# Optimization experiments

Hardware: AMD Instinct MI355X
Metric: run time of the kernel (lower is better)

Reference implementation:

```python
import jax, jax.numpy as jnp
import numpy as np
import math

N_HEAD = 8
LN_EPS = 1e-5


def _layernorm(x, w, b):
    # Biased variance as in the triton kernel: var = E[x^2] - mean^2
    mean = jnp.mean(x, axis=-1, keepdims=True)
    var = jnp.mean(x * x, axis=-1, keepdims=True) - mean * mean
    return (x - mean) * jax.lax.rsqrt(var + LN_EPS) * w + b


def _gelu_tanh(x):
    # matches triton gelu: tanh approximation
    return 0.5 * x * (1.0 + jnp.tanh(0.7978845608 * (x + 0.044715 * x * x * x)))


def _causal_attention(qkv, n_head):
    B, T, C3 = qkv.shape
    C = C3 // 3
    D = C // n_head
    q, k, v = jnp.split(qkv, 3, axis=-1)
    q = q.reshape(B, T, n_head, D)
    k = k.reshape(B, T, n_head, D)
    v = v.reshape(B, T, n_head, D)
    scale = 1.0 / math.sqrt(D)
    scores = jnp.einsum('bqhd,bkhd->bhqk', q, k) * scale  # [B,H,T,T]
    causal = jnp.tril(jnp.ones((T, T), dtype=bool))
    scores = jnp.where(causal, scores, -jnp.inf)
    p = jax.nn.softmax(scores, axis=-1)
    out = jnp.einsum('bhqk,bkhd->bqhd', p, v)
    return out.reshape(B, T, C)


def setup_inputs() -> dict:
    key = jax.random.key(0)
    ks = jax.random.split(key, 8)
    B, T, C = 8, 2048, 768
    s = 0.02
    return {
        'x': jax.random.normal(ks[0], (B, T, C), jnp.float32),
        'ln1_w': jnp.ones((C,), jnp.float32),
        'ln1_b': jnp.zeros((C,), jnp.float32),
        'w_qkv': jax.random.normal(ks[1], (3 * C, C), jnp.float32) * s,
        'b_qkv': jnp.zeros((3 * C,), jnp.float32),
        'w_attn_proj': jax.random.normal(ks[2], (C, C), jnp.float32) * s,
        'b_attn_proj': jnp.zeros((C,), jnp.float32),
        'ln2_w': jnp.ones((C,), jnp.float32),
        'ln2_b': jnp.zeros((C,), jnp.float32),
        'w_fc': jax.random.normal(ks[3], (4 * C, C), jnp.float32) * s,
        'b_fc': jnp.zeros((4 * C,), jnp.float32),
        'w_mlp_proj': jax.random.normal(ks[4], (C, 4 * C), jnp.float32) * s,
        'b_mlp_proj': jnp.zeros((C,), jnp.float32),
    }


def reference(x, ln1_w, ln1_b, w_qkv, b_qkv, w_attn_proj, b_attn_proj,
              ln2_w, ln2_b, w_fc, b_fc, w_mlp_proj, b_mlp_proj):
    # attention block: fused LN + QKV linear, causal flash attention, out proj, residual
    qkv = _layernorm(x, ln1_w, ln1_b) @ w_qkv.T + b_qkv          # [B,T,3C]
    att = _causal_attention(qkv, N_HEAD)                          # [B,T,C]
    x = x + (att @ w_attn_proj.T + b_attn_proj)
    # MLP block: fused LN + fc + gelu, proj, residual
    h = _gelu_tanh(_layernorm(x, ln2_w, ln2_b) @ w_fc.T + b_fc)   # [B,T,4C]
    x = x + (h @ w_mlp_proj.T + b_mlp_proj)
    return x
```

## Files before the change

kernel.cpp:

```cpp
#include <hip/hip_runtime.h>
#include <hip/hip_bf16.h>
#include <cstdint>
#include <cstddef>

typedef __attribute__((ext_vector_type(8))) short bf16x8;
typedef __attribute__((ext_vector_type(4))) short bf16x4;
typedef __attribute__((ext_vector_type(4))) float f32x4;
typedef __attribute__((ext_vector_type(16))) float f32x16;

#define GLB_AS(p) ((const __attribute__((address_space(1))) void*)(p))
#define LDS_AS(p) ((__attribute__((address_space(3))) void*)(p))

__device__ __forceinline__ short f2bf(float f) {
    union { float f; unsigned u; } x; x.f = f;
    unsigned r = (x.u + 0x7fffu + ((x.u >> 16) & 1u)) >> 16;
    return (short)r;
}
__device__ __forceinline__ float bf2f(short s) {
    union { unsigned u; float f; } x;
    x.u = ((unsigned)(unsigned short)s) << 16;
    return x.f;
}
__device__ __forceinline__ unsigned packbf2(float a, float b) {
    union { float f; unsigned u; } x, y; x.f = a; y.f = b;
    return (x.u >> 16) | (y.u & 0xffff0000u);
}
__device__ __forceinline__ f32x4 MF(bf16x8 a, bf16x8 b, f32x4 c) {
    return __builtin_amdgcn_mfma_f32_16x16x32_bf16(a, b, c, 0, 0, 0);
}
__device__ __forceinline__ f32x16 MF32(bf16x8 a, bf16x8 b, f32x16 c) {
    return __builtin_amdgcn_mfma_f32_32x32x16_bf16(a, b, c, 0, 0, 0);
}

__global__ __launch_bounds__(256) void k_prep(const float* __restrict__ x,
                                              const float* __restrict__ ln1_w,
                                              const float* __restrict__ ln1_b,
                                              short* __restrict__ xhat,
                                              const float* __restrict__ s0,
                                              const float* __restrict__ s1,
                                              const float* __restrict__ s2,
                                              const float* __restrict__ s3,
                                              short* __restrict__ d0,
                                              short* __restrict__ d1,
                                              short* __restrict__ d2,
                                              short* __restrict__ d3,
                                              int n0, int n1, int n2, int n3) {
    const int row = blockIdx.x;
    const int tid = threadIdx.x;
    {
        const float* xr = x + (size_t)row * 768;
        float v0 = xr[tid], v1 = xr[tid + 256], v2 = xr[tid + 512];
        float s = v0 + v1 + v2;
        float ss = v0 * v0 + v1 * v1 + v2 * v2;
        #pragma unroll
        for (int m = 32; m; m >>= 1) { s += __shfl_xor(s, m); ss += __shfl_xor(ss, m); }
        __shared__ float red[8];
        int wid = tid >> 6, lane = tid & 63;
        if (lane == 0) { red[wid] = s; red[4 + wid] = ss; }
        __syncthreads();
        s = red[0] + red[1] + red[2] + red[3];
        ss = red[4] + red[5] + red[6] + red[7];
        float mean = s * (1.f / 768.f);
        float var = ss * (1.f / 768.f) - mean * mean;
        float inv = rsqrtf(var + 1e-5f);
        short* orow = xhat + (size_t)row * 768;
        orow[tid]       = f2bf((v0 - mean) * inv * ln1_w[tid]       + ln1_b[tid]);
        orow[tid + 256] = f2bf((v1 - mean) * inv * ln1_w[tid + 256] + ln1_b[tid + 256]);
        orow[tid + 512] = f2bf((v2 - mean) * inv * ln1_w[tid + 512] + ln1_b[tid + 512]);
    }
    const int total = n0 + n1 + n2 + n3;
    const int stride = gridDim.x * 256;
    for (int i = blockIdx.x * 256 + tid; i < total; i += stride) {
        int j = i;
        const float* s; short* d;
        if (j < n0) { s = s0; d = d0; }
        else {
            j -= n0;
            if (j < n1) { s = s1; d = d1; }
            else {
                j -= n1;
                if (j < n2) { s = s2; d = d2; }
                else { j -= n2; s = s3; d = d3; }
            }
        }
        float4 v = ((const float4*)s)[j];
        bf16x4 o;
        o[0] = f2bf(v.x); o[1] = f2bf(v.y); o[2] = f2bf(v.z); o[3] = f2bf(v.w);
        ((bf16x4*)d)[j] = o;
    }
}

__global__ __launch_bounds__(256) void k_layernorm_bf(const short* __restrict__ xb,
                                                      const float* __restrict__ w,
                                                      const float* __restrict__ b,
                                                      short* __restrict__ out) {
    const int row = blockIdx.x;
    const int tid = threadIdx.x;
    float v[4] = {0.f, 0.f, 0.f, 0.f};
    if (tid < 192) {
        bf16x4 raw = ((const bf16x4*)(xb + (size_t)row * 768))[tid];
        #pragma unroll
        for (int j = 0; j < 4; ++j) v[j] = bf2f(raw[j]);
    }
    float s = v[0] + v[1] + v[2] + v[3];
    float ss = v[0] * v[0] + v[1] * v[1] + v[2] * v[2] + v[3] * v[3];
    #pragma unroll
    for (int m = 32; m; m >>= 1) { s += __shfl_xor(s, m); ss += __shfl_xor(ss, m); }
    __shared__ float red[8];
    int wid = tid >> 6, lane = tid & 63;
    if (lane == 0) { red[wid] = s; red[4 + wid] = ss; }
    __syncthreads();
    s = red[0] + red[1] + red[2] + red[3];
    ss = red[4] + red[5] + red[6] + red[7];
    float mean = s * (1.f / 768.f);
    float var = ss * (1.f / 768.f) - mean * mean;
    float inv = rsqrtf(var + 1e-5f);
    if (tid < 192) {
        float4 wv = ((const float4*)w)[tid];
        float4 bv = ((const float4*)b)[tid];
        bf16x4 o;
        o[0] = f2bf((v[0] - mean) * inv * wv.x + bv.x);
        o[1] = f2bf((v[1] - mean) * inv * wv.y + bv.y);
        o[2] = f2bf((v[2] - mean) * inv * wv.z + bv.z);
        o[3] = f2bf((v[3] - mean) * inv * wv.w + bv.w);
        ((bf16x4*)(out + (size_t)row * 768))[tid] = o;
    }
}

template <int EPI, int NFR>
__global__ __launch_bounds__(512, 2) void k_gemm256(const short* __restrict__ A,
                                                    const short* __restrict__ B,
                                                    const float* __restrict__ bias,
                                                    const void* __restrict__ res,
                                                    void* __restrict__ out,
                                                    int M, int N, int K) {
    __shared__ short As2[2][256 * 64];
    __shared__ short Bs2[2][NFR * 64 * 64];
    const int tid = threadIdx.x, lane = tid & 63, wid = tid >> 6;
    const int l4 = lane & 15, lh = lane >> 4;
    const int wm = wid >> 2, wn = wid & 3;
    const int gx = gridDim.x;
    const int nwg = gx * gridDim.y;
    int wg = blockIdx.y * gx + blockIdx.x;
    { const int q = nwg >> 3; wg = (wg & 7) * q + (wg >> 3); }
    const int row0 = (wg / gx) * 256, col0 = (wg % gx) * (NFR * 64);

    auto stageA = [&](short* lds, int mh, int k0) {
        #pragma unroll
        for (int i = 0; i < 2; ++i) {
            const int chunk = wid * 2 + i;
            const int dl = mh * 16384 + chunk * 1024 + lane * 16;
            const int r = dl >> 7;
            const int cb = (dl & 127) ^ ((r & 7) << 4);
            __builtin_amdgcn_global_load_lds(
                GLB_AS(A + (size_t)(row0 + r) * K + k0 + (cb >> 1)),
                LDS_AS(lds + mh * 8192 + chunk * 512), 16, 0, 0);
        }
    };
    auto stageB = [&](short* lds, int k0) {
        #pragma unroll
        for (int i = 0; i < NFR; ++i) {
            const int chunk = wid * NFR + i;
            const int dl = chunk * 1024 + lane * 16;
            const int r = dl >> 7;
            const int cb = (dl & 127) ^ ((r & 7) << 4);
            __builtin_amdgcn_global_load_lds(
                GLB_AS(B + (size_t)(col0 + r) * K + k0 + (cb >> 1)),
                LDS_AS(lds + chunk * 512), 16, 0, 0);
        }
    };
    auto rd = [&](const short* lds, int r, int kb) -> bf16x8 {
        return *(const bf16x8*)((const char*)lds + r * 128 +
                                ((kb * 64 + lh * 16) ^ ((r & 7) << 4)));
    };

    f32x4 acc[8][NFR] = {};
    bf16x8 a[4][2], b0[2][2], b1[2][2];
    const int NT = K >> 6;

    stageA(As2[0], 0, 0);
    stageA(As2[0], 1, 0);
    stageB(Bs2[0], 0);
    asm volatile("s_waitcnt vmcnt(0)" ::: "memory");
    __builtin_amdgcn_s_barrier();

    for (int t = 0; t < NT; ++t) {
        const int cur = t & 1, nxt = cur ^ 1;
        const short* Ac = As2[cur];
        const short* Bc = Bs2[cur];
        const int kn = (t + 1) << 6;
        const bool more = (t + 1 < NT);
        #pragma unroll
        for (int mi = 0; mi < 4; ++mi) {
            const int r = wm * 128 + mi * 16 + l4;
            a[mi][0] = rd(Ac, r, 0); a[mi][1] = rd(Ac, r, 1);
        }
        #pragma unroll
        for (int ni = 0; ni < 2; ++ni) {
            const int r = wn * (NFR * 16) + ni * 16 + l4;
            b0[ni][0] = rd(Bc, r, 0); b0[ni][1] = rd(Bc, r, 1);
        }
        if (more) { stageA(As2[nxt], 0, kn); stageA(As2[nxt], 1, kn); }
        __builtin_amdgcn_s_setprio(1);
        #pragma unroll
        for (int mi = 0; mi < 4; ++mi)
            #pragma unroll
            for (int ni = 0; ni < 2; ++ni) {
                acc[mi][ni] = MF(a[mi][0], b0[ni][0], acc[mi][ni]);
                acc[mi][ni] = MF(a[mi][1], b0[ni][1], acc[mi][ni]);
            }
        __builtin_amdgcn_s_setprio(0);
        __builtin_amdgcn_s_barrier();
        #pragma unroll
        for (int j = 0; j < NFR - 2; ++j) {
            const int r = wn * (NFR * 16) + (2 + j) * 16 + l4;
            b1[j][0] = rd(Bc, r, 0); b1[j][1] = rd(Bc, r, 1);
        }
        if (more) stageB(Bs2[nxt], kn);
        __builtin_amdgcn_s_setprio(1);
        #pragma unroll
        for (int mi = 0; mi < 4; ++mi)
            #pragma unroll
            for (int j = 0; j < NFR - 2; ++j) {
                acc[mi][2 + j] = MF(a[mi][0], b1[j][0], acc[mi][2 + j]);
                acc[mi][2 + j] = MF(a[mi][1], b1[j][1], acc[mi][2 + j]);
            }
        __builtin_amdgcn_s_setprio(0);
        __builtin_amdgcn_s_barrier();
        #pragma unroll
        for (int mi = 0; mi < 4; ++mi) {
            const int r = wm * 128 + (4 + mi) * 16 + l4;
            a[mi][0] = rd(Ac, r, 0); a[mi][1] = rd(Ac, r, 1);
        }
        __builtin_amdgcn_s_setprio(1);
        #pragma unroll
        for (int mi = 0; mi < 4; ++mi)
            #pragma unroll
            for (int j = 0; j < NFR - 2; ++j) {
                acc[4 + mi][2 + j] = MF(a[mi][0], b1[j][0], acc[4 + mi][2 + j]);
                acc[4 + mi][2 + j] = MF(a[mi][1], b1[j][1], acc[4 + mi][2 + j]);
            }
        __builtin_amdgcn_s_setprio(0);
        __builtin_amdgcn_s_barrier();
        __builtin_amdgcn_s_setprio(1);
        #pragma unroll
        for (int mi = 0; mi < 4; ++mi)
            #pragma unroll
            for (int ni = 0; ni < 2; ++ni) {
                acc[4 + mi][ni] = MF(a[mi][0], b0[ni][0], acc[4 + mi][ni]);
                acc[4 + mi][ni] = MF(a[mi][1], b0[ni][1], acc[4 + mi][ni]);
            }
        __builtin_amdgcn_s_setprio(0);
        if (more) asm volatile("s_waitcnt vmcnt(0)" ::: "memory");
        __builtin_amdgcn_s_barrier();
    }

    #pragma unroll
    for (int mi = 0; mi < 8; ++mi) {
        const int rowb = row0 + wm * 128 + mi * 16 + lh * 4;
        #pragma unroll
        for (int ni = 0; ni < NFR; ++ni) {
            const int col = col0 + wn * (NFR * 16) + ni * 16 + l4;
            const float bv = bias[col];
            #pragma unroll
            for (int j = 0; j < 4; ++j) {
                const size_t idx = (size_t)(rowb + j) * N + col;
                float v = acc[mi][ni][j] + bv;
                if (EPI == 0) {
                    ((short*)out)[idx] = f2bf(v);
                } else if (EPI == 2) {
                    float u = v + 0.044715f * v * v * v;
                    float t = 1.f - 2.f / (__expf(1.5957691216f * u) + 1.f);
                    ((short*)out)[idx] = f2bf(0.5f * v * (1.f + t));
                } else if (EPI == 3) {
                    ((short*)out)[idx] = f2bf(v + ((const float*)res)[idx]);
                } else {
                    ((float*)out)[idx] = v + bf2f(((const short*)res)[idx]);
                }
            }
        }
    }
}

#define ATTN_PROC(QF, O, LROW, QA, Q0)                                         \
    if (kv0 <= (Q0) + 31) {                                                    \
        const bool full = (kv0 + 63 <= (Q0));                                  \
        f32x16 s0 = {}, s1 = {};                                               \
        __builtin_amdgcn_s_setprio(1);                                         \
        _Pragma("unroll")                                                      \
        for (int kb = 0; kb < 6; ++kb) {                                       \
            const int r0 = lq, r1 = 32 + lq;                                   \
            bf16x8 kf0 = *(const bf16x8*)((const char*)&Ks[cur][0] +           \
                          r0 * 256 + ((kb * 32 + hi * 16) ^ ((r0 & 7) << 4))); \
            bf16x8 kf1 = *(const bf16x8*)((const char*)&Ks[cur][0] +           \
                          r1 * 256 + ((kb * 32 + hi * 16) ^ ((r1 & 7) << 4))); \
            s0 = MF32(kf0, QF[kb], s0);                                        \
            s1 = MF32(kf1, QF[kb], s1);                                        \
        }                                                                      \
        __builtin_amdgcn_s_setprio(0);                                         \
        if (!full) {                                                           \
            _Pragma("unroll")                                                  \
            for (int r = 0; r < 16; ++r) {                                     \
                const int kvl = (r & 3) + 8 * (r >> 2) + 4 * hi;               \
                if (kv0 + kvl > (QA)) s0[r] = -INFINITY;                       \
                if (kv0 + 32 + kvl > (QA)) s1[r] = -INFINITY;                  \
            }                                                                  \
        }                                                                      \
        _Pragma("unroll")                                                      \
        for (int r = 0; r < 16; ++r) { s0[r] = exp2f(s0[r]); s1[r] = exp2f(s1[r]); } \
        float ar[16];                                                          \
        _Pragma("unroll")                                                      \
        for (int r = 0; r < 16; ++r) ar[r] = s0[r] + s1[r];                    \
        _Pragma("unroll")                                                      \
        for (int st = 8; st; st >>= 1)                                         \
            _Pragma("unroll")                                                  \
            for (int r = 0; r < 8; ++r)                                        \
                if (r < st) ar[r] += ar[r + st];                               \
        (LROW) += ar[0] + __shfl_xor(ar[0], 32);                               \
        unsigned pk0[8], pk1[8];                                               \
        _Pragma("unroll")                                                      \
        for (int j = 0; j < 8; ++j) {                                          \
            pk0[j] = packbf2(s0[2 * j], s0[2 * j + 1]);                        \
            pk1[j] = packbf2(s1[2 * j], s1[2 * j + 1]);                        \
        }                                                                      \
        __builtin_amdgcn_s_setprio(1);                                         \
        _Pragma("unroll")                                                      \
        for (int db = 0; db < 3; ++db) {                                       \
            const int vrow = db * 32 + lq;                                     \
            const int vsw = ((vrow & 7) ^ ((vrow >> 3) & 7)) << 4;             \
            _Pragma("unroll")                                                  \
            for (int c = 0; c < 4; ++c) {                                      \
                bf16x8 vf = *(const bf16x8*)((const char*)&Vs[cur][0] +        \
                             vrow * 128 + ((c * 32 + hi * 16) ^ vsw));         \
                union { unsigned u[4]; bf16x8 v; } pa;                         \
                const unsigned* pk = (c < 2) ? pk0 : pk1;                      \
                const int o4 = (c & 1) * 4;                                    \
                pa.u[0] = pk[o4]; pa.u[1] = pk[o4 + 1];                        \
                pa.u[2] = pk[o4 + 2]; pa.u[3] = pk[o4 + 3];                    \
                (O)[db] = MF32(vf, pa.v, (O)[db]);                             \
            }                                                                  \
        }                                                                      \
        __builtin_amdgcn_s_setprio(0);                                         \
    }

__global__ __launch_bounds__(256, 2) void k_attn8(const short* __restrict__ qkv,
                                                  short* __restrict__ att) {
    __shared__ short Ks[2][64 * 128];
    __shared__ short Vs[2][96 * 64];
    const int tid = threadIdx.x, lane = tid & 63, wid = tid >> 6;
    const int lq = lane & 31, hi = lane >> 5;
    const int L = blockIdx.x;
    const int h = L & 7, bx = (L >> 3) & 7, b = L >> 6;
    const short* base = qkv + (size_t)b * 2048 * 2304 + h * 96;
    const short* Kb = base + 768;
    const short* Vb = base + 1536;
    const int vkvr = (tid / 12) * 4, vd0 = (tid % 12) * 8;
    const int vslot = (vkvr & ~12) | ((vkvr & 4) << 1) | ((vkvr & 8) >> 1);
    bf16x8 vreg[4];
    const float QSC = 0.14724445f;

    auto stageK = [&](int jt, int bb) {
        const int kv0 = jt * 64;
        for (int c = wid; c < 16; c += 4) {
            const int dl = c * 1024 + lane * 16;
            const int row = dl >> 8;
            const int scol = (dl & 255) ^ ((row & 7) << 4);
            __builtin_amdgcn_global_load_lds(GLB_AS(Kb + (size_t)(kv0 + row) * 2304 + (scol >> 1)),
                                             LDS_AS(&Ks[bb][c * 512]), 16, 0, 0);
        }
    };
    auto loadV = [&](int jt) {
        if (tid < 192) {
            const int kv0 = jt * 64;
            #pragma unroll
            for (int e = 0; e < 4; ++e)
                vreg[e] = *(const bf16x8*)(Vb + (size_t)(kv0 + vkvr + e) * 2304 + vd0);
        }
    };
    auto writeV = [&](int bb) {
        if (tid < 192) {
            #pragma unroll
            for (int f = 0; f < 8; ++f) {
                const int row = vd0 + f;
                const int sw = ((row & 7) ^ ((row >> 3) & 7)) << 4;
                const int byte = (row * 128 + vslot * 2) ^ sw;
                bf16x4 w4;
                w4[0] = vreg[0][f]; w4[1] = vreg[1][f]; w4[2] = vreg[2][f]; w4[3] = vreg[3][f];
                *(bf16x4*)((char*)&Vs[bb][0] + byte) = w4;
            }
        }
    };

    const int qtH = 15 - bx, qtL = bx;
    const int q0H = qtH * 128 + wid * 32, q0L = qtL * 128 + wid * 32;
    const int qaH = q0H + lq, qaL = q0L + lq;

    bf16x8 qfH[6], qfL[6];
    #pragma unroll
    for (int kb = 0; kb < 6; ++kb) {
        bf16x8 vH = *(const bf16x8*)(base + (size_t)qaH * 2304 + kb * 16 + hi * 8);
        bf16x8 vL = *(const bf16x8*)(base + (size_t)qaL * 2304 + kb * 16 + hi * 8);
        #pragma unroll
        for (int e = 0; e < 8; ++e) {
            qfH[kb][e] = f2bf(bf2f(vH[e]) * QSC);
            qfL[kb][e] = f2bf(bf2f(vL[e]) * QSC);
        }
    }

    f32x16 oH[3] = {}, oL[3] = {};
    float lrowH = 0.f, lrowL = 0.f;
    const int nt = 2 * qtH + 2;

    stageK(0, 0);
    loadV(0);
    asm volatile("s_waitcnt vmcnt(0)" ::: "memory");
    writeV(0);
    __syncthreads();

    int cur = 0;
    for (int jt = 0; jt < nt; ++jt) {
        const int nxt = cur ^ 1;
        const bool more = (jt + 1 < nt);
        if (more) { stageK(jt + 1, nxt); loadV(jt + 1); }

        const int kv0 = jt * 64;
        ATTN_PROC(qfH, oH, lrowH, qaH, q0H)
        ATTN_PROC(qfL, oL, lrowL, qaL, q0L)

        if (more) {
            asm volatile("s_waitcnt vmcnt(0)" ::: "memory");
            writeV(nxt);
        }
        __syncthreads();
        cur = nxt;
    }

    {
        const float inv = 1.f / lrowH;
        short* orow = att + (size_t)((size_t)b * 2048 + qaH) * 768 + h * 96;
        #pragma unroll
        for (int db = 0; db < 3; ++db)
            #pragma unroll
            for (int j = 0; j < 4; ++j) {
                bf16x4 ov;
                #pragma unroll
                for (int e = 0; e < 4; ++e) ov[e] = f2bf(oH[db][4 * j + e] * inv);
                *(bf16x4*)(orow + db * 32 + 8 * j + 4 * hi) = ov;
            }
    }
    {
        const float inv = 1.f / lrowL;
        short* orow = att + (size_t)((size_t)b * 2048 + qaL) * 768 + h * 96;
        #pragma unroll
        for (int db = 0; db < 3; ++db)
            #pragma unroll
            for (int j = 0; j < 4; ++j) {
                bf16x4 ov;
                #pragma unroll
                for (int e = 0; e < 4; ++e) ov[e] = f2bf(oL[db][4 * j + e] * inv);
                *(bf16x4*)(orow + db * 32 + 8 * j + 4 * hi) = ov;
            }
    }
}

extern "C" void kernel_launch(void* const* d_in, const int* in_sizes, int n_in,
                              void* d_out, int out_size, void* d_ws, size_t ws_size,
                              hipStream_t stream) {
    (void)in_sizes; (void)n_in; (void)out_size; (void)ws_size;
    const float* x      = (const float*)d_in[0];
    const float* ln1_w  = (const float*)d_in[1];
    const float* ln1_b  = (const float*)d_in[2];
    const float* w_qkv  = (const float*)d_in[3];
    const float* b_qkv  = (const float*)d_in[4];
    const float* w_proj = (const float*)d_in[5];
    const float* b_proj = (const float*)d_in[6];
    const float* ln2_w  = (const float*)d_in[7];
    const float* ln2_b  = (const float*)d_in[8];
    const float* w_fc   = (const float*)d_in[9];
    const float* b_fc   = (const float*)d_in[10];
    const float* w_mlp  = (const float*)d_in[11];
    const float* b_mlp  = (const float*)d_in[12];

    const int C = 768, M = 8 * 2048;

    char* ws = (char*)d_ws;
    size_t off = 0;
    auto alloc = [&](size_t bytes) {
        char* p = ws + off;
        off += (bytes + 255) & ~(size_t)255;
        return p;
    };
    short* wqkv_b = (short*)alloc((size_t)3 * C * C * 2);
    short* wproj_b = (short*)alloc((size_t)C * C * 2);
    short* wfc_b  = (short*)alloc((size_t)4 * C * C * 2);
    short* wmlp_b = (short*)alloc((size_t)4 * C * C * 2);
    short* bufA   = (short*)alloc((size_t)M * C * 2);
    short* bufB   = (short*)alloc((size_t)M * 4 * C * 2);
    short* x2b    = (short*)alloc((size_t)M * C * 2);

    k_prep<<<dim3(M), dim3(256), 0, stream>>>(
        x, ln1_w, ln1_b, bufA,
        w_qkv, w_proj, w_fc, w_mlp, wqkv_b, wproj_b, wfc_b, wmlp_b,
        3 * C * C / 4, C * C / 4, 4 * C * C / 4, 4 * C * C / 4);

    k_gemm256<0, 3><<<dim3(2304 / 192, M / 256), dim3(512), 0, stream>>>(
        bufA, wqkv_b, b_qkv, nullptr, bufB, M, 2304, C);
    k_attn8<<<dim3(512), dim3(256), 0, stream>>>(bufB, bufA);
    k_gemm256<3, 3><<<dim3(768 / 192, M / 256), dim3(512), 0, stream>>>(
        bufA, wproj_b, b_proj, x, x2b, M, C, C);
    k_layernorm_bf<<<dim3(M), dim3(256), 0, stream>>>(x2b, ln2_w, ln2_b, bufA);
    k_gemm256<2, 4><<<dim3(3072 / 256, M / 256), dim3(512), 0, stream>>>(
        bufA, wfc_b, b_fc, nullptr, bufB, M, 3072, C);
    k_gemm256<4, 3><<<dim3(768 / 192, M / 256), dim3(512), 0, stream>>>(
        bufB, wmlp_b, b_mlp, x2b, d_out, M, C, 4 * C);
}
```

Measured before the change: 411.6 us.

## Add 256x384-tile GEMM kernel for the MLP fc layer

Adds a k_gemm384 kernel that computes a 256x384 output tile per 512-thread workgroup and uses it for the LN2→fc→GELU GEMM in place of the 256x256 tile. The grid shrinks from 768 to 512 workgroups, which is exactly two waves over 256 CUs. The wider tile is meant to raise operand reuse per LDS load and reduce tail imbalance. In exchange it needs 160KB of double-buffered LDS and 192 accumulator floats per lane, which limits occupancy to one workgroup per CU and risks register spills.

```diff
diff --git a/kernel.cpp b/kernel.cpp
--- a/kernel.cpp
+++ b/kernel.cpp
@@ -261,6 +261,175 @@
         #pragma unroll
         for (int ni = 0; ni < NFR; ++ni) {
             const int col = col0 + wn * (NFR * 16) + ni * 16 + l4;
+            const float bv = bias[col];
+            #pragma unroll
+            for (int j = 0; j < 4; ++j) {
+                const size_t idx = (size_t)(rowb + j) * N + col;
+                float v = acc[mi][ni][j] + bv;
+                if (EPI == 0) {
+                    ((short*)out)[idx] = f2bf(v);
+                } else if (EPI == 2) {
+                    float u = v + 0.044715f * v * v * v;
+                    float t = 1.f - 2.f / (__expf(1.5957691216f * u) + 1.f);
+                    ((short*)out)[idx] = f2bf(0.5f * v * (1.f + t));
+                } else if (EPI == 3) {
+                    ((short*)out)[idx] = f2bf(v + ((const float*)res)[idx]);
+                } else {
+                    ((float*)out)[idx] = v + bf2f(((const short*)res)[idx]);
+                }
+            }
+        }
+    }
+}
+
+template <int EPI>
+__global__ __launch_bounds__(512, 2) void k_gemm384(const short* __restrict__ A,
+                                                    const short* __restrict__ B,
+                                                    const float* __restrict__ bias,
+                                                    const void* __restrict__ res,
+                                                    void* __restrict__ out,
+                                                    int M, int N, int K) {
+    __shared__ short As2[2][256 * 64];
+    __shared__ short Bs2[2][384 * 64];
+    const int tid = threadIdx.x, lane = tid & 63, wid = tid >> 6;
+    const int l4 = lane & 15, lh = lane >> 4;
+    const int wm = wid >> 2, wn = wid & 3;
+    const int gx = gridDim.x;
+    const int nwg = gx * gridDim.y;
+    int wg = blockIdx.y * gx + blockIdx.x;
+    { const int q = nwg >> 3; wg = (wg & 7) * q + (wg >> 3); }
+    const int row0 = (wg / gx) * 256, col0 = (wg % gx) * 384;
+
+    auto stageA = [&](short* lds, int mh, int k0) {
+        #pragma unroll
+        for (int i = 0; i < 2; ++i) {
+            const int chunk = wid * 2 + i;
+            const int dl = mh * 16384 + chunk * 1024 + lane * 16;
+            const int r = dl >> 7;
+            const int cb = (dl & 127) ^ ((r & 7) << 4);
+            __builtin_amdgcn_global_load_lds(
+                GLB_AS(A + (size_t)(row0 + r) * K + k0 + (cb >> 1)),
+                LDS_AS(lds + mh * 8192 + chunk * 512), 16, 0, 0);
+        }
+    };
+    auto stageB = [&](short* lds, int k0) {
+        #pragma unroll
+        for (int i = 0; i < 6; ++i) {
+            const int chunk = wid * 6 + i;
+            const int dl = chunk * 1024 + lane * 16;
+            const int r = dl >> 7;
+            const int cb = (dl & 127) ^ ((r & 7) << 4);
+            __builtin_amdgcn_global_load_lds(
+                GLB_AS(B + (size_t)(col0 + r) * K + k0 + (cb >> 1)),
+                LDS_AS(lds + chunk * 512), 16, 0, 0);
+        }
+    };
+    auto rd = [&](const short* lds, int r, int kb) -> bf16x8 {
+        return *(const bf16x8*)((const char*)lds + r * 128 +
+                                ((kb * 64 + lh * 16) ^ ((r & 7) << 4)));
+    };
+
+    f32x4 acc[8][6] = {};
+    const int NT = K >> 6;
+
+    stageA(As2[0], 0, 0);
+    stageA(As2[0], 1, 0);
+    stageB(Bs2[0], 0);
+    asm volatile("s_waitcnt vmcnt(0)" ::: "memory");
+    __builtin_amdgcn_s_barrier();
+
+    for (int t = 0; t < NT; ++t) {
+        const int cur = t & 1, nxt = cur ^ 1;
+        const short* Ac = As2[cur];
+        const short* Bc = Bs2[cur];
+        const int kn = (t + 1) << 6;
+        const bool more = (t + 1 < NT);
+        bf16x8 a[4][2];
+        {
+            bf16x8 b0[3][2];
+            #pragma unroll
+            for (int mi = 0; mi < 4; ++mi) {
+                const int r = wm * 128 + mi * 16 + l4;
+                a[mi][0] = rd(Ac, r, 0); a[mi][1] = rd(Ac, r, 1);
+            }
+            #pragma unroll
+            for (int ni = 0; ni < 3; ++ni) {
+                const int r = wn * 96 + ni * 16 + l4;
+                b0[ni][0] = rd(Bc, r, 0); b0[ni][1] = rd(Bc, r, 1);
+            }
+            if (more) { stageA(As2[nxt], 0, kn); stageA(As2[nxt], 1, kn); }
+            __builtin_amdgcn_s_setprio(1);
+            #pragma unroll
+            for (int mi = 0; mi < 4; ++mi)
+                #pragma unroll
+                for (int ni = 0; ni < 3; ++ni) {
+                    acc[mi][ni] = MF(a[mi][0], b0[ni][0], acc[mi][ni]);
+                    acc[mi][ni] = MF(a[mi][1], b0[ni][1], acc[mi][ni]);
+                }
+            __builtin_amdgcn_s_setprio(0);
+        }
+        __builtin_amdgcn_s_barrier();
+        {
+            bf16x8 b1[3][2];
+            #pragma unroll
+            for (int j = 0; j < 3; ++j) {
+                const int r = wn * 96 + (3 + j) * 16 + l4;
+                b1[j][0] = rd(Bc, r, 0); b1[j][1] = rd(Bc, r, 1);
+            }
+            if (more) stageB(Bs2[nxt], kn);
+            __builtin_amdgcn_s_setprio(1);
+            #pragma unroll
+            for (int mi = 0; mi < 4; ++mi)
+                #pragma unroll
+                for (int j = 0; j < 3; ++j) {
+                    acc[mi][3 + j] = MF(a[mi][0], b1[j][0], acc[mi][3 + j]);
+                    acc[mi][3 + j] = MF(a[mi][1], b1[j][1], acc[mi][3 + j]);
+                }
+            __builtin_amdgcn_s_setprio(0);
+            __builtin_amdgcn_s_barrier();
+            #pragma unroll
+            for (int mi = 0; mi < 4; ++mi) {
+                const int r = wm * 128 + (4 + mi) * 16 + l4;
+                a[mi][0] = rd(Ac, r, 0); a[mi][1] = rd(Ac, r, 1);
+            }
+            __builtin_amdgcn_s_setprio(1);
+            #pragma unroll
+            for (int mi = 0; mi < 4; ++mi)
+                #pragma unroll
+                for (int j = 0; j < 3; ++j) {
+                    acc[4 + mi][3 + j] = MF(a[mi][0], b1[j][0], acc[4 + mi][3 + j]);
+                    acc[4 + mi][3 + j] = MF(a[mi][1], b1[j][1], acc[4 + mi][3 + j]);
+                }
+            __builtin_amdgcn_s_setprio(0);
+        }
+        __builtin_amdgcn_s_barrier();
+        {
+            bf16x8 b0b[3][2];
+            #pragma unroll
+            for (int ni = 0; ni < 3; ++ni) {
+                const int r = wn * 96 + ni * 16 + l4;
+                b0b[ni][0] = rd(Bc, r, 0); b0b[ni][1] = rd(Bc, r, 1);
+            }
+            __builtin_amdgcn_s_setprio(1);
+            #pragma unroll
+            for (int mi = 0; mi < 4; ++mi)
+                #pragma unroll
+                for (int ni = 0; ni < 3; ++ni) {
+                    acc[4 + mi][ni] = MF(a[mi][0], b0b[ni][0], acc[4 + mi][ni]);
+                    acc[4 + mi][ni] = MF(a[mi][1], b0b[ni][1], acc[4 + mi][ni]);
+                }
+            __builtin_amdgcn_s_setprio(0);
+        }
+        if (more) asm volatile("s_waitcnt vmcnt(0)" ::: "memory");
+        __builtin_amdgcn_s_barrier();
+    }
+
+    #pragma unroll
+    for (int mi = 0; mi < 8; ++mi) {
+        const int rowb = row0 + wm * 128 + mi * 16 + lh * 4;
+        #pragma unroll
+        for (int ni = 0; ni < 6; ++ni) {
+            const int col = col0 + wn * 96 + ni * 16 + l4;
             const float bv = bias[col];
             #pragma unroll
             for (int j = 0; j < 4; ++j) {
@@ -509,7 +678,7 @@
     k_gemm256<3, 3><<<dim3(768 / 192, M / 256), dim3(512), 0, stream>>>(
         bufA, wproj_b, b_proj, x, x2b, M, C, C);
     k_layernorm_bf<<<dim3(M), dim3(256), 0, stream>>>(x2b, ln2_w, ln2_b, bufA);
-    k_gemm256<2, 4><<<dim3(3072 / 256, M / 256), dim3(512), 0, stream>>>(
+    k_gemm384<2><<<dim3(3072 / 384, M / 256), dim3(512), 0, stream>>>(
         bufA, wfc_b, b_fc, nullptr, bufB, M, 3072, C);
     k_gemm256<4, 3><<<dim3(768 / 192, M / 256), dim3(512), 0, stream>>>(
         bufB, wmlp_b, b_mlp, x2b, d_out, M, C, 4 * C);
```

New measurement: 512.5 us. 1.25x slower.
